# Performance work log

Hardware: AMD Instinct MI355X
Metric: run time of the kernel (lower is better)

The kernel has to match this reference:

```python
import jax, jax.numpy as jnp
import numpy as np

NUM_HEADS = 8
NEG_MASK = -1000.0  # original code masks with -1000, not -inf


def setup_inputs() -> dict:
    key = jax.random.key(0)
    ks = jax.random.split(key, 12)
    B, S, D = 4, 2048, 512
    HID, OUT = 512, 512
    dh = D // NUM_HEADS      # 64, per-head input dim
    eh = HID // NUM_HEADS    # 64, per-head hidden dim
    w = 0.02
    return {
        "q": jax.random.normal(ks[0], (B, S, D), dtype=jnp.float32),
        "k": jax.random.normal(ks[1], (B, S, D), dtype=jnp.float32),
        "v": jax.random.normal(ks[2], (B, S, D), dtype=jnp.float32),
        # Linear weights stored as [in, out] (transpose of torch convention)
        "Wq": jax.random.normal(ks[3], (dh, eh), dtype=jnp.float32) * w,
        "bq": jax.random.normal(ks[4], (eh,), dtype=jnp.float32) * w,
        "Wk": jax.random.normal(ks[5], (dh, eh), dtype=jnp.float32) * w,
        "bk": jax.random.normal(ks[6], (eh,), dtype=jnp.float32) * w,
        "Wv": jax.random.normal(ks[7], (dh, eh), dtype=jnp.float32) * w,
        "bv": jax.random.normal(ks[8], (eh,), dtype=jnp.float32) * w,
        "Wo": jax.random.normal(ks[9], (HID, OUT), dtype=jnp.float32) * w,
        "bo": jax.random.normal(ks[10], (OUT,), dtype=jnp.float32) * w,
        "valid_lens": jnp.maximum(jax.random.randint(ks[11], (B,), 0, S), 1),
        "max_len": S,
    }


def reference(q, k, v, Wq, bq, Wk, bk, Wv, bv, Wo, bo, valid_lens, max_len):
    B, S, D = q.shape
    H = NUM_HEADS
    # split into heads: [B, S, H, dh]; note the SAME projection weights are
    # shared across heads (as in the original module)
    qh = q.reshape(B, S, H, D // H)
    kh = k.reshape(B, S, H, D // H)
    vh = v.reshape(B, S, H, D // H)
    qp = jnp.einsum('bshd,de->bshe', qh, Wq) + bq  # [B,S,H,eh]
    kp = jnp.einsum('bshd,de->bshe', kh, Wk) + bk
    vp = jnp.einsum('bshd,de->bshe', vh, Wv) + bv
    scale = 1.0 / jnp.sqrt(jnp.asarray(qp.shape[-1], qp.dtype))
    scores = jnp.einsum('bshe,bthe->bhst', qp, kp) * scale  # [B,H,S,S]
    # key-padding mask: positions j >= valid_len get -1000 (original semantics)
    key_mask = jnp.arange(S)[None, :] < valid_lens[:, None]  # [B,S]
    scores = jnp.where(key_mask[:, None, None, :], scores, NEG_MASK)
    attn = jax.nn.softmax(scores, axis=-1)
    ctx = jnp.einsum('bhst,bthe->bshe', attn, vp).reshape(B, S, -1)  # head-major concat
    return jnp.einsum('bse,eo->bso', ctx, Wo) + bo
```

## Files before the change

kernel.cpp:

```cpp
#include <hip/hip_runtime.h>

#define S_LEN 2048
#define D_MODEL 512

typedef __attribute__((ext_vector_type(8))) short s8v;
typedef __attribute__((ext_vector_type(4))) float f4v;
typedef __attribute__((ext_vector_type(4))) short s4v;
typedef __attribute__((ext_vector_type(4))) int   i4v;
typedef __attribute__((ext_vector_type(2))) int   i2v;

#define MFMA __builtin_amdgcn_mfma_f32_16x16x32_bf16

__device__ inline short f2bf(float x) {
    union { float f; unsigned u; } v; v.f = x;
    unsigned r = v.u + 0x7fffu + ((v.u >> 16) & 1u);
    return (short)(r >> 16);
}
__device__ inline unsigned pack_bf2_trunc(float a, float b) {
    unsigned ua = __builtin_bit_cast(unsigned, a);
    unsigned ub = __builtin_bit_cast(unsigned, b);
    return (ua >> 16) | (ub & 0xffff0000u);
}

template <int C>
__device__ inline float dppf(float x) {
    int i = __builtin_bit_cast(int, x);
    i = __builtin_amdgcn_update_dpp(0, i, C, 0xF, 0xF, true);
    return __builtin_bit_cast(float, i);
}
__device__ inline float rowsum16(float x) {
    x += dppf<0xB1>(x);
    x += dppf<0x4E>(x);
    x += dppf<0x141>(x);
    x += dppf<0x140>(x);
    return x;
}

typedef const __attribute__((address_space(1))) void* gptr_t;
typedef __attribute__((address_space(3))) void* sptr_t;
__device__ inline void gload16(const void* g, void* s) {
    __builtin_amdgcn_global_load_lds((gptr_t)g, (sptr_t)s, 16, 0, 0);
}

__global__ __launch_bounds__(256) void prep_kernel(
    const float* __restrict__ Wo, short* __restrict__ WoT)
{
    __shared__ short t[64 * 65];
    const int bi = (blockIdx.x >> 3) * 64;
    const int bj = (blockIdx.x & 7) * 64;
    const int c = threadIdx.x & 63, rr = threadIdx.x >> 6;
#pragma unroll
    for (int r = 0; r < 16; r++) {
        int i = r * 4 + rr;
        t[c * 65 + i] = f2bf(Wo[(size_t)(bi + i) * 512 + bj + c]);
    }
    __syncthreads();
#pragma unroll
    for (int r = 0; r < 16; r++) {
        int o = r * 4 + rr;
        WoT[(size_t)(bj + o) * 512 + bi + c] = t[o * 65 + c];
    }
}

__global__ __launch_bounds__(256) void proj_kernel(
    const float* __restrict__ q, const float* __restrict__ k, const float* __restrict__ v,
    const float* __restrict__ Wq, const float* __restrict__ Wk, const float* __restrict__ Wv,
    const float* __restrict__ bq, const float* __restrict__ bk, const float* __restrict__ bv,
    short* __restrict__ qp, short* __restrict__ kfrag, short* __restrict__ vfrag)
{
    __shared__ short sm[128 * 64];

    const int t = blockIdx.z >> 2;
    const int b = blockIdx.z & 3;
    const int h = blockIdx.y;
    const int qt = blockIdx.x;
    const int w = threadIdx.x >> 6, lane = threadIdx.x & 63;
    const int l = lane & 15, qd = lane >> 4;

    const float* X    = (t == 0) ? q  : (t == 1) ? k  : v;
    const float* Wp   = (t == 0) ? Wq : (t == 1) ? Wk : Wv;
    const float* bias = (t == 0) ? bq : (t == 1) ? bk : bv;

    {
        const int d = threadIdx.x >> 2, c4 = threadIdx.x & 3;
        const float* src = Wp + d * 64 + c4 * 16;
        f4v x0 = *(const f4v*)(src);
        f4v x1 = *(const f4v*)(src + 4);
        f4v x2 = *(const f4v*)(src + 8);
        f4v x3 = *(const f4v*)(src + 12);
        float xs[16] = {x0[0],x0[1],x0[2],x0[3], x1[0],x1[1],x1[2],x1[3],
                        x2[0],x2[1],x2[2],x2[3], x3[0],x3[1],x3[2],x3[3]};
#pragma unroll
        for (int j = 0; j < 16; j++) {
            int e = c4 * 16 + j;
            int sidx = (e * 64 + d) ^ (((e >> 2) & 7) << 3);
            sm[sidx] = f2bf(xs[j]);
        }
    }
    __syncthreads();

    const int s0 = qt * 128 + w * 32;

    s8v a[2][2];
#pragma unroll
    for (int mt = 0; mt < 2; mt++)
#pragma unroll
        for (int kk = 0; kk < 2; kk++) {
            const float* p = X + (size_t)(b * S_LEN + s0 + mt * 16 + l) * 512 + h * 64 + kk * 32 + qd * 8;
            f4v x0 = *(const f4v*)p;
            f4v x1 = *(const f4v*)(p + 4);
            s8v fr;
            fr[0] = f2bf(x0[0]); fr[1] = f2bf(x0[1]); fr[2] = f2bf(x0[2]); fr[3] = f2bf(x0[3]);
            fr[4] = f2bf(x1[0]); fr[5] = f2bf(x1[1]); fr[6] = f2bf(x1[2]); fr[7] = f2bf(x1[3]);
            a[mt][kk] = fr;
        }
    s8v wf[4][2];
#pragma unroll
    for (int nt = 0; nt < 4; nt++) {
        int wrow = (t < 2) ? (4 * l + nt) : (nt * 16 + l);
        int key = ((wrow >> 2) & 7) << 3;
#pragma unroll
        for (int kk = 0; kk < 2; kk++)
            wf[nt][kk] = *(const s8v*)(sm + ((wrow * 64 + kk * 32 + qd * 8) ^ key));
    }

    const f4v fz = {0.f, 0.f, 0.f, 0.f};
    f4v acc[2][4];
#pragma unroll
    for (int mt = 0; mt < 2; mt++)
#pragma unroll
        for (int nt = 0; nt < 4; nt++) acc[mt][nt] = fz;

#pragma unroll
    for (int kk = 0; kk < 2; kk++)
#pragma unroll
        for (int nt = 0; nt < 4; nt++)
#pragma unroll
            for (int mt = 0; mt < 2; mt++)
                acc[mt][nt] = MFMA(a[mt][kk], wf[nt][kk], acc[mt][nt], 0, 0, 0);

    const float SC = 0.125f * 1.442695041f;

    if (t == 0) {
        float bbs[4];
#pragma unroll
        for (int nt = 0; nt < 4; nt++) bbs[nt] = bias[4 * l + nt];
#pragma unroll
        for (int mt = 0; mt < 2; mt++)
#pragma unroll
            for (int r = 0; r < 4; r++) {
                int s = s0 + mt * 16 + qd * 4 + r;
                s4v pk;
#pragma unroll
                for (int nt = 0; nt < 4; nt++)
                    pk[nt] = f2bf((acc[mt][nt][r] + bbs[nt]) * SC);
                *(s4v*)(qp + ((size_t)(b * 8 + h) * S_LEN + s) * 64 + 4 * l) = pk;
            }
        return;
    }

    __syncthreads();

    if (t == 1) {
        float bbs[4];
#pragma unroll
        for (int nt = 0; nt < 4; nt++) bbs[nt] = bias[4 * l + nt];
#pragma unroll
        for (int mt = 0; mt < 2; mt++)
#pragma unroll
            for (int r = 0; r < 4; r++) {
                int sl = w * 32 + mt * 16 + qd * 4 + r;
                s4v pk;
#pragma unroll
                for (int nt = 0; nt < 4; nt++) pk[nt] = f2bf(acc[mt][nt][r] + bbs[nt]);
                int sidx = (sl * 64 + 4 * l) ^ (((sl >> 2) & 7) << 3);
                *(s4v*)(sm + sidx) = pk;
            }
    } else {
#pragma unroll
        for (int nt = 0; nt < 4; nt++) {
            float bb = bias[nt * 16 + l];
            int e = nt * 16 + l;
            int key = ((e >> 2) & 7) << 3;
#pragma unroll
            for (int mt = 0; mt < 2; mt++) {
                s4v pk;
#pragma unroll
                for (int r = 0; r < 4; r++) pk[r] = f2bf(acc[mt][nt][r] + bb);
                int sidx = (e * 128 + w * 32 + mt * 16 + qd * 4) ^ key;
                *(s4v*)(sm + sidx) = pk;
            }
        }
    }
    __syncthreads();

    short* dst = (t == 1) ? kfrag : vfrag;
    const size_t obase0 = ((size_t)(b * 8 + h) * 32 + qt * 2) * 4096;
    const int f = threadIdx.x & 63, cp = threadIdx.x >> 6;
    const int fl = f & 15, fq = f >> 4;
#pragma unroll
    for (int tt = 0; tt < 2; tt++)
#pragma unroll
        for (int ci = 0; ci < 2; ci++) {
            int c = cp + ci * 4;
            int n2 = c >> 1, kk = c & 1;
            int sidx;
            if (t == 1) {
                int sl = tt * 64 + 4 * fl + n2;
                sidx = (sl * 64 + kk * 32 + fq * 8) ^ (((sl >> 2) & 7) << 3);
            } else {
                int e = 4 * fl + n2;
                sidx = (e * 128 + tt * 64 + kk * 32 + fq * 8) ^ (((e >> 2) & 7) << 3);
            }
            s8v x = *(const s8v*)(sm + sidx);
            *(s8v*)(dst + obase0 + tt * 4096 + c * 512 + f * 8) = x;
        }
}

__global__ __launch_bounds__(256, 3) void attn_kernel(
    const short* __restrict__ qp, const short* __restrict__ kfrag,
    const short* __restrict__ vfrag,
    const int* __restrict__ valid_lens, short* __restrict__ ctx)
{
    __shared__ alignas(16) short kbuf[2][4096];
    __shared__ alignas(16) short lP[4][32 * 72];

    const int gid = blockIdx.x;
    const int h  = gid & 7;
    int b        = (gid >> 3) & 3;
    const int qt = gid >> 5;
    b ^= 3 * ((gid >> 8) & 1);
    const int w = threadIdx.x >> 6, lane = threadIdx.x & 63;
    const int l = lane & 15, qd = lane >> 4;
    const int vlen = valid_lens[b];
    const int ntiles = (vlen + 63) >> 6;

    const int bh = b * 8 + h;
    const short* Qs = qp + (size_t)bh * S_LEN * 64;
    const short* Kf = kfrag + (size_t)bh * 32 * 4096;
    const short* Vf = vfrag + (size_t)bh * 32 * 4096;

    const int s0 = qt * 128 + w * 32;
    s8v qf[2][2];
#pragma unroll
    for (int mt = 0; mt < 2; mt++)
#pragma unroll
        for (int kk = 0; kk < 2; kk++)
            qf[mt][kk] = *(const s8v*)(Qs + (size_t)(s0 + mt * 16 + l) * 64 + kk * 32 + qd * 8);

    const f4v fz = {0.f, 0.f, 0.f, 0.f};
    f4v O[2][4];
    float lsum[2][4];
#pragma unroll
    for (int mt = 0; mt < 2; mt++)
#pragma unroll
        for (int r = 0; r < 4; r++) lsum[mt][r] = 0.f;
#pragma unroll
    for (int mt = 0; mt < 2; mt++)
#pragma unroll
        for (int ne = 0; ne < 4; ne++) O[mt][ne] = fz;

    short* lPw = lP[w];
    const int toff = threadIdx.x * 8;

    gload16(Kf + toff,        &kbuf[0][toff]);
    gload16(Kf + 2048 + toff, &kbuf[0][2048 + toff]);
    __syncthreads();

    for (int kb = 0; kb < ntiles; kb++) {
        const int cur = kb & 1;
        if (kb + 1 < ntiles) {
            const short* Ks = Kf + (size_t)(kb + 1) * 4096;
            gload16(Ks + toff,        &kbuf[cur ^ 1][toff]);
            gload16(Ks + 2048 + toff, &kbuf[cur ^ 1][2048 + toff]);
        }

        const short* Vb = Vf + (size_t)kb * 4096 + lane * 8;
        s8v vf[4][2];
#pragma unroll
        for (int ne = 0; ne < 4; ne++)
#pragma unroll
            for (int kk = 0; kk < 2; kk++)
                vf[ne][kk] = *(const s8v*)(Vb + (ne * 2 + kk) * 512);

        const short* Kb = &kbuf[cur][lane * 8];
        s8v kf[4][2];
#pragma unroll
        for (int nt = 0; nt < 4; nt++)
#pragma unroll
            for (int kk = 0; kk < 2; kk++)
                kf[nt][kk] = *(const s8v*)(Kb + (nt * 2 + kk) * 512);

        f4v sf[2][4];
#pragma unroll
        for (int mt = 0; mt < 2; mt++)
#pragma unroll
            for (int nt = 0; nt < 4; nt++) sf[mt][nt] = fz;
        __builtin_amdgcn_s_setprio(1);
#pragma unroll
        for (int nt = 0; nt < 4; nt++)
#pragma unroll
            for (int mt = 0; mt < 2; mt++) {
                sf[mt][nt] = MFMA(qf[mt][0], kf[nt][0], sf[mt][nt], 0, 0, 0);
                sf[mt][nt] = MFMA(qf[mt][1], kf[nt][1], sf[mt][nt], 0, 0, 0);
            }
        __builtin_amdgcn_s_setprio(0);

        if (kb == ntiles - 1 && (vlen & 63)) {
            int rem = vlen - kb * 64;
#pragma unroll
            for (int nt = 0; nt < 4; nt++)
                if (4 * l + nt >= rem) {
#pragma unroll
                    for (int mt = 0; mt < 2; mt++)
#pragma unroll
                        for (int r = 0; r < 4; r++) sf[mt][nt][r] = -1e30f;
                }
        }

#pragma unroll
        for (int mt = 0; mt < 2; mt++)
#pragma unroll
            for (int r = 0; r < 4; r++) {
                float p0 = __builtin_amdgcn_exp2f(sf[mt][0][r]);
                float p1 = __builtin_amdgcn_exp2f(sf[mt][1][r]);
                float p2 = __builtin_amdgcn_exp2f(sf[mt][2][r]);
                float p3 = __builtin_amdgcn_exp2f(sf[mt][3][r]);
                lsum[mt][r] += (p0 + p1) + (p2 + p3);
                i2v pk;
                pk[0] = (int)pack_bf2_trunc(p0, p1);
                pk[1] = (int)pack_bf2_trunc(p2, p3);
                *(i2v*)(lPw + (mt * 16 + qd * 4 + r) * 72 + 4 * l) = pk;
            }

        s8v pa[2][2];
#pragma unroll
        for (int mt = 0; mt < 2; mt++)
#pragma unroll
            for (int kk = 0; kk < 2; kk++)
                pa[mt][kk] = *(const s8v*)(lPw + (mt * 16 + l) * 72 + kk * 32 + qd * 8);
        __builtin_amdgcn_s_setprio(1);
#pragma unroll
        for (int ne = 0; ne < 4; ne++)
#pragma unroll
            for (int mt = 0; mt < 2; mt++) {
                O[mt][ne] = MFMA(pa[mt][0], vf[ne][0], O[mt][ne], 0, 0, 0);
                O[mt][ne] = MFMA(pa[mt][1], vf[ne][1], O[mt][ne], 0, 0, 0);
            }
        __builtin_amdgcn_s_setprio(0);

        __syncthreads();
    }

#pragma unroll
    for (int mt = 0; mt < 2; mt++)
#pragma unroll
        for (int r = 0; r < 4; r++) {
            float inv = 1.0f / rowsum16(lsum[mt][r]);
            int s = s0 + mt * 16 + qd * 4 + r;
            s4v pk;
#pragma unroll
            for (int ne = 0; ne < 4; ne++) pk[ne] = f2bf(O[mt][ne][r] * inv);
            *(s4v*)(ctx + ((size_t)(b * S_LEN + s)) * 512 + h * 64 + 4 * l) = pk;
        }
}

__global__ __launch_bounds__(256) void outproj_kernel(
    const short* __restrict__ ctx, const short* __restrict__ WoT,
    const float* __restrict__ bo, float* __restrict__ out)
{
    __shared__ short lB[64 * 520];
    __shared__ short lA[128 * 40];

    const int rb = blockIdx.x * 128;
    const int nb = blockIdx.y * 64;
    const int w = threadIdx.x >> 6, lane = threadIdx.x & 63;
    const int l = lane & 15, qd = lane >> 4;

    {
        int n = threadIdx.x >> 2, c0 = threadIdx.x & 3;
#pragma unroll
        for (int i = 0; i < 16; i++) {
            int g = i * 4 + c0;
            i4v x = *(const i4v*)(WoT + (size_t)(nb + n) * 512 + g * 8);
            *(i4v*)(lB + n * 520 + g * 8) = x;
        }
    }
    __syncthreads();

    const f4v fz = {0.f, 0.f, 0.f, 0.f};
    f4v acc[2][4];
#pragma unroll
    for (int mt = 0; mt < 2; mt++)
#pragma unroll
        for (int nt = 0; nt < 4; nt++) acc[mt][nt] = fz;

    for (int ko = 0; ko < 16; ko++) {
        {
            int r = threadIdx.x >> 1, hp = threadIdx.x & 1;
            const short* src = ctx + (size_t)(rb + r) * 512 + ko * 32 + hp * 16;
            i4v x0 = *(const i4v*)src;
            i4v x1 = *(const i4v*)(src + 8);
            *(i4v*)(lA + r * 40 + hp * 16) = x0;
            *(i4v*)(lA + r * 40 + hp * 16 + 8) = x1;
        }
        __syncthreads();
        s8v af[2];
#pragma unroll
        for (int mt = 0; mt < 2; mt++)
            af[mt] = *(const s8v*)(lA + (w * 32 + mt * 16 + l) * 40 + qd * 8);
#pragma unroll
        for (int nt = 0; nt < 4; nt++) {
            s8v bfr = *(const s8v*)(lB + (nt * 16 + l) * 520 + ko * 32 + qd * 8);
#pragma unroll
            for (int mt = 0; mt < 2; mt++)
                acc[mt][nt] = MFMA(af[mt], bfr, acc[mt][nt], 0, 0, 0);
        }
        __syncthreads();
    }

#pragma unroll
    for (int nt = 0; nt < 4; nt++) {
        float bias = bo[nb + nt * 16 + l];
#pragma unroll
        for (int mt = 0; mt < 2; mt++)
#pragma unroll
            for (int r = 0; r < 4; r++) {
                int row = rb + w * 32 + mt * 16 + qd * 4 + r;
                out[(size_t)row * 512 + nb + nt * 16 + l] = acc[mt][nt][r] + bias;
            }
    }
}

extern "C" void kernel_launch(void* const* d_in, const int* in_sizes, int n_in,
                              void* d_out, int out_size, void* d_ws, size_t ws_size,
                              hipStream_t stream)
{
    const float* q  = (const float*)d_in[0];
    const float* k  = (const float*)d_in[1];
    const float* v  = (const float*)d_in[2];
    const float* Wq = (const float*)d_in[3];
    const float* bq = (const float*)d_in[4];
    const float* Wk = (const float*)d_in[5];
    const float* bk = (const float*)d_in[6];
    const float* Wv = (const float*)d_in[7];
    const float* bv = (const float*)d_in[8];
    const float* Wo = (const float*)d_in[9];
    const float* bo = (const float*)d_in[10];
    const int*   vl = (const int*)d_in[11];
    float* out = (float*)d_out;

    char* ws = (char*)d_ws;
    const size_t SL = (size_t)4 * 8 * S_LEN * 64 * sizeof(short);
    short* qp    = (short*)(ws);
    short* ctx   = (short*)(ws + SL);
    short* kfrag = (short*)(ws + 2 * SL);
    short* vfrag = (short*)(ws + 3 * SL);
    short* WoT   = (short*)(ws + 4 * SL);

    prep_kernel<<<64, 256, 0, stream>>>(Wo, WoT);
    proj_kernel<<<dim3(16, 8, 12), 256, 0, stream>>>(q, k, v, Wq, Wk, Wv,
                                                     bq, bk, bv, qp, kfrag, vfrag);
    attn_kernel<<<512, 256, 0, stream>>>(qp, kfrag, vfrag, vl, ctx);
    outproj_kernel<<<dim3(64, 8), 256, 0, stream>>>(ctx, WoT, bo, out);
}
```

Measured before the change: 167.5 us.

## Software-pipeline PV MFMA one tile behind QK with double-buffered P

Restructures the attention loop so the P·V MFMAs for the previous key tile are issued together with the current tile's QK^T MFMAs. The P tile is double-buffered in shared memory per wave, and a tail step handles the last tile. V fragments are loaded after the MFMAs, so they are in flight during the exp/softmax step. Occupancy hint drops from 3 to 2 blocks per CU to make room for the extra live registers and LDS, which trades parallelism for instruction-level overlap.

```diff
diff --git a/kernel.cpp b/kernel.cpp
--- a/kernel.cpp
+++ b/kernel.cpp
@@ -217,13 +217,13 @@
         }
 }
 
-__global__ __launch_bounds__(256, 3) void attn_kernel(
+__global__ __launch_bounds__(256, 2) void attn_kernel(
     const short* __restrict__ qp, const short* __restrict__ kfrag,
     const short* __restrict__ vfrag,
     const int* __restrict__ valid_lens, short* __restrict__ ctx)
 {
     __shared__ alignas(16) short kbuf[2][4096];
-    __shared__ alignas(16) short lP[4][32 * 72];
+    __shared__ alignas(16) short lP[4][2][32 * 72];
 
     const int gid = blockIdx.x;
     const int h  = gid & 7;
@@ -260,12 +260,13 @@
 #pragma unroll
         for (int ne = 0; ne < 4; ne++) O[mt][ne] = fz;
 
-    short* lPw = lP[w];
     const int toff = threadIdx.x * 8;
 
     gload16(Kf + toff,        &kbuf[0][toff]);
     gload16(Kf + 2048 + toff, &kbuf[0][2048 + toff]);
     __syncthreads();
+
+    s8v vf[4][2];
 
     for (int kb = 0; kb < ntiles; kb++) {
         const int cur = kb & 1;
@@ -275,14 +276,6 @@
             gload16(Ks + 2048 + toff, &kbuf[cur ^ 1][2048 + toff]);
         }
 
-        const short* Vb = Vf + (size_t)kb * 4096 + lane * 8;
-        s8v vf[4][2];
-#pragma unroll
-        for (int ne = 0; ne < 4; ne++)
-#pragma unroll
-            for (int kk = 0; kk < 2; kk++)
-                vf[ne][kk] = *(const s8v*)(Vb + (ne * 2 + kk) * 512);
-
         const short* Kb = &kbuf[cur][lane * 8];
         s8v kf[4][2];
 #pragma unroll
@@ -290,6 +283,16 @@
 #pragma unroll
             for (int kk = 0; kk < 2; kk++)
                 kf[nt][kk] = *(const s8v*)(Kb + (nt * 2 + kk) * 512);
+
+        s8v pa[2][2];
+        if (kb > 0) {
+            const short* lPr = lP[w][cur ^ 1];
+#pragma unroll
+            for (int mt = 0; mt < 2; mt++)
+#pragma unroll
+                for (int kk = 0; kk < 2; kk++)
+                    pa[mt][kk] = *(const s8v*)(lPr + (mt * 16 + l) * 72 + kk * 32 + qd * 8);
+        }
 
         f4v sf[2][4];
 #pragma unroll
@@ -304,7 +307,23 @@
                 sf[mt][nt] = MFMA(qf[mt][0], kf[nt][0], sf[mt][nt], 0, 0, 0);
                 sf[mt][nt] = MFMA(qf[mt][1], kf[nt][1], sf[mt][nt], 0, 0, 0);
             }
+        if (kb > 0) {
+#pragma unroll
+            for (int ne = 0; ne < 4; ne++)
+#pragma unroll
+                for (int mt = 0; mt < 2; mt++) {
+                    O[mt][ne] = MFMA(pa[mt][0], vf[ne][0], O[mt][ne], 0, 0, 0);
+                    O[mt][ne] = MFMA(pa[mt][1], vf[ne][1], O[mt][ne], 0, 0, 0);
+                }
+        }
         __builtin_amdgcn_s_setprio(0);
+
+        const short* Vb = Vf + (size_t)kb * 4096 + lane * 8;
+#pragma unroll
+        for (int ne = 0; ne < 4; ne++)
+#pragma unroll
+            for (int kk = 0; kk < 2; kk++)
+                vf[ne][kk] = *(const s8v*)(Vb + (ne * 2 + kk) * 512);
 
         if (kb == ntiles - 1 && (vlen & 63)) {
             int rem = vlen - kb * 64;
@@ -318,28 +337,35 @@
                 }
         }
 
-#pragma unroll
-        for (int mt = 0; mt < 2; mt++)
-#pragma unroll
-            for (int r = 0; r < 4; r++) {
-                float p0 = __builtin_amdgcn_exp2f(sf[mt][0][r]);
-                float p1 = __builtin_amdgcn_exp2f(sf[mt][1][r]);
-                float p2 = __builtin_amdgcn_exp2f(sf[mt][2][r]);
-                float p3 = __builtin_amdgcn_exp2f(sf[mt][3][r]);
-                lsum[mt][r] += (p0 + p1) + (p2 + p3);
-                i2v pk;
-                pk[0] = (int)pack_bf2_trunc(p0, p1);
-                pk[1] = (int)pack_bf2_trunc(p2, p3);
-                *(i2v*)(lPw + (mt * 16 + qd * 4 + r) * 72 + 4 * l) = pk;
-            }
-
+        {
+            short* lPwr = lP[w][cur];
+#pragma unroll
+            for (int mt = 0; mt < 2; mt++)
+#pragma unroll
+                for (int r = 0; r < 4; r++) {
+                    float p0 = __builtin_amdgcn_exp2f(sf[mt][0][r]);
+                    float p1 = __builtin_amdgcn_exp2f(sf[mt][1][r]);
+                    float p2 = __builtin_amdgcn_exp2f(sf[mt][2][r]);
+                    float p3 = __builtin_amdgcn_exp2f(sf[mt][3][r]);
+                    lsum[mt][r] += (p0 + p1) + (p2 + p3);
+                    i2v pk;
+                    pk[0] = (int)pack_bf2_trunc(p0, p1);
+                    pk[1] = (int)pack_bf2_trunc(p2, p3);
+                    *(i2v*)(lPwr + (mt * 16 + qd * 4 + r) * 72 + 4 * l) = pk;
+                }
+        }
+
+        __syncthreads();
+    }
+
+    {
+        const short* lPr = lP[w][(ntiles - 1) & 1];
         s8v pa[2][2];
 #pragma unroll
         for (int mt = 0; mt < 2; mt++)
 #pragma unroll
             for (int kk = 0; kk < 2; kk++)
-                pa[mt][kk] = *(const s8v*)(lPw + (mt * 16 + l) * 72 + kk * 32 + qd * 8);
-        __builtin_amdgcn_s_setprio(1);
+                pa[mt][kk] = *(const s8v*)(lPr + (mt * 16 + l) * 72 + kk * 32 + qd * 8);
 #pragma unroll
         for (int ne = 0; ne < 4; ne++)
 #pragma unroll
@@ -347,9 +373,6 @@
                 O[mt][ne] = MFMA(pa[mt][0], vf[ne][0], O[mt][ne], 0, 0, 0);
                 O[mt][ne] = MFMA(pa[mt][1], vf[ne][1], O[mt][ne], 0, 0, 0);
             }
-        __builtin_amdgcn_s_setprio(0);
-
-        __syncthreads();
     }
 
 #pragma unroll
```

New measurement: 168.8 us. Within noise of the previous version (+0.8%).

## Process two 64-key subtiles per barrier with 128-key double-buffered K staging

Applied to the files above, without the earlier changes.

The attention loop now stages 128 keys of K per pipeline step instead of 64 and runs two 64-key subtiles between each pair of __syncthreads, which halves the number of block-wide barriers and K prefetch rounds. The LDS K buffer doubles in size, and occupancy bounds drop from 3 to 2 blocks per CU. Masking of the tail subtile moves to the last outer iteration. A subtile past vlen can still be processed when vlen rounds to an odd count of 64-key tiles. It is fully masked, so it adds wasted work and possible out-of-range K/V reads.

```diff
diff --git a/kernel.cpp b/kernel.cpp
--- a/kernel.cpp
+++ b/kernel.cpp
@@ -217,12 +217,12 @@
         }
 }
 
-__global__ __launch_bounds__(256, 3) void attn_kernel(
+__global__ __launch_bounds__(256, 2) void attn_kernel(
     const short* __restrict__ qp, const short* __restrict__ kfrag,
     const short* __restrict__ vfrag,
     const int* __restrict__ valid_lens, short* __restrict__ ctx)
 {
-    __shared__ alignas(16) short kbuf[2][4096];
+    __shared__ alignas(16) short kbuf[2][8192];
     __shared__ alignas(16) short lP[4][32 * 72];
 
     const int gid = blockIdx.x;
@@ -233,7 +233,7 @@
     const int w = threadIdx.x >> 6, lane = threadIdx.x & 63;
     const int l = lane & 15, qd = lane >> 4;
     const int vlen = valid_lens[b];
-    const int ntiles = (vlen + 63) >> 6;
+    const int nt2 = (vlen + 127) >> 7;
 
     const int bh = b * 8 + h;
     const short* Qs = qp + (size_t)bh * S_LEN * 64;
@@ -263,91 +263,100 @@
     short* lPw = lP[w];
     const int toff = threadIdx.x * 8;
 
-    gload16(Kf + toff,        &kbuf[0][toff]);
-    gload16(Kf + 2048 + toff, &kbuf[0][2048 + toff]);
-    __syncthreads();
-
-    for (int kb = 0; kb < ntiles; kb++) {
-        const int cur = kb & 1;
-        if (kb + 1 < ntiles) {
-            const short* Ks = Kf + (size_t)(kb + 1) * 4096;
-            gload16(Ks + toff,        &kbuf[cur ^ 1][toff]);
-            gload16(Ks + 2048 + toff, &kbuf[cur ^ 1][2048 + toff]);
-        }
-
-        const short* Vb = Vf + (size_t)kb * 4096 + lane * 8;
-        s8v vf[4][2];
-#pragma unroll
-        for (int ne = 0; ne < 4; ne++)
-#pragma unroll
-            for (int kk = 0; kk < 2; kk++)
-                vf[ne][kk] = *(const s8v*)(Vb + (ne * 2 + kk) * 512);
-
-        const short* Kb = &kbuf[cur][lane * 8];
-        s8v kf[4][2];
-#pragma unroll
-        for (int nt = 0; nt < 4; nt++)
-#pragma unroll
-            for (int kk = 0; kk < 2; kk++)
-                kf[nt][kk] = *(const s8v*)(Kb + (nt * 2 + kk) * 512);
-
-        f4v sf[2][4];
-#pragma unroll
-        for (int mt = 0; mt < 2; mt++)
-#pragma unroll
-            for (int nt = 0; nt < 4; nt++) sf[mt][nt] = fz;
-        __builtin_amdgcn_s_setprio(1);
-#pragma unroll
-        for (int nt = 0; nt < 4; nt++)
-#pragma unroll
-            for (int mt = 0; mt < 2; mt++) {
-                sf[mt][nt] = MFMA(qf[mt][0], kf[nt][0], sf[mt][nt], 0, 0, 0);
-                sf[mt][nt] = MFMA(qf[mt][1], kf[nt][1], sf[mt][nt], 0, 0, 0);
-            }
-        __builtin_amdgcn_s_setprio(0);
-
-        if (kb == ntiles - 1 && (vlen & 63)) {
-            int rem = vlen - kb * 64;
+#pragma unroll
+    for (int r = 0; r < 4; r++)
+        gload16(Kf + r * 2048 + toff, &kbuf[0][r * 2048 + toff]);
+    __syncthreads();
+
+    for (int j = 0; j < nt2; j++) {
+        const int cur = j & 1;
+        if (j + 1 < nt2) {
+            const short* Ks = Kf + (size_t)(j + 1) * 8192;
+#pragma unroll
+            for (int r = 0; r < 4; r++)
+                gload16(Ks + r * 2048 + toff, &kbuf[cur ^ 1][r * 2048 + toff]);
+        }
+
+#pragma unroll
+        for (int st = 0; st < 2; st++) {
+            const int kb = 2 * j + st;
+
+            const short* Vb = Vf + (size_t)kb * 4096 + lane * 8;
+            s8v vf[4][2];
+#pragma unroll
+            for (int ne = 0; ne < 4; ne++)
+#pragma unroll
+                for (int kk = 0; kk < 2; kk++)
+                    vf[ne][kk] = *(const s8v*)(Vb + (ne * 2 + kk) * 512);
+
+            const short* Kb = &kbuf[cur][st * 4096 + lane * 8];
+            s8v kf[4][2];
 #pragma unroll
             for (int nt = 0; nt < 4; nt++)
-                if (4 * l + nt >= rem) {
-#pragma unroll
-                    for (int mt = 0; mt < 2; mt++)
-#pragma unroll
-                        for (int r = 0; r < 4; r++) sf[mt][nt][r] = -1e30f;
+#pragma unroll
+                for (int kk = 0; kk < 2; kk++)
+                    kf[nt][kk] = *(const s8v*)(Kb + (nt * 2 + kk) * 512);
+
+            f4v sf[2][4];
+#pragma unroll
+            for (int mt = 0; mt < 2; mt++)
+#pragma unroll
+                for (int nt = 0; nt < 4; nt++) sf[mt][nt] = fz;
+            __builtin_amdgcn_s_setprio(1);
+#pragma unroll
+            for (int nt = 0; nt < 4; nt++)
+#pragma unroll
+                for (int mt = 0; mt < 2; mt++) {
+                    sf[mt][nt] = MFMA(qf[mt][0], kf[nt][0], sf[mt][nt], 0, 0, 0);
+                    sf[mt][nt] = MFMA(qf[mt][1], kf[nt][1], sf[mt][nt], 0, 0, 0);
                 }
-        }
-
-#pragma unroll
-        for (int mt = 0; mt < 2; mt++)
-#pragma unroll
-            for (int r = 0; r < 4; r++) {
-                float p0 = __builtin_amdgcn_exp2f(sf[mt][0][r]);
-                float p1 = __builtin_amdgcn_exp2f(sf[mt][1][r]);
-                float p2 = __builtin_amdgcn_exp2f(sf[mt][2][r]);
-                float p3 = __builtin_amdgcn_exp2f(sf[mt][3][r]);
-                lsum[mt][r] += (p0 + p1) + (p2 + p3);
-                i2v pk;
-                pk[0] = (int)pack_bf2_trunc(p0, p1);
-                pk[1] = (int)pack_bf2_trunc(p2, p3);
-                *(i2v*)(lPw + (mt * 16 + qd * 4 + r) * 72 + 4 * l) = pk;
-            }
-
-        s8v pa[2][2];
-#pragma unroll
-        for (int mt = 0; mt < 2; mt++)
-#pragma unroll
-            for (int kk = 0; kk < 2; kk++)
-                pa[mt][kk] = *(const s8v*)(lPw + (mt * 16 + l) * 72 + kk * 32 + qd * 8);
-        __builtin_amdgcn_s_setprio(1);
-#pragma unroll
-        for (int ne = 0; ne < 4; ne++)
-#pragma unroll
-            for (int mt = 0; mt < 2; mt++) {
-                O[mt][ne] = MFMA(pa[mt][0], vf[ne][0], O[mt][ne], 0, 0, 0);
-                O[mt][ne] = MFMA(pa[mt][1], vf[ne][1], O[mt][ne], 0, 0, 0);
-            }
-        __builtin_amdgcn_s_setprio(0);
+            __builtin_amdgcn_s_setprio(0);
+
+            if (j == nt2 - 1) {
+                int rem = vlen - kb * 64;
+                if (rem < 64) {
+#pragma unroll
+                    for (int nt = 0; nt < 4; nt++)
+                        if (4 * l + nt >= rem) {
+#pragma unroll
+                            for (int mt = 0; mt < 2; mt++)
+#pragma unroll
+                                for (int r = 0; r < 4; r++) sf[mt][nt][r] = -1e30f;
+                        }
+                }
+            }
+
+#pragma unroll
+            for (int mt = 0; mt < 2; mt++)
+#pragma unroll
+                for (int r = 0; r < 4; r++) {
+                    float p0 = __builtin_amdgcn_exp2f(sf[mt][0][r]);
+                    float p1 = __builtin_amdgcn_exp2f(sf[mt][1][r]);
+                    float p2 = __builtin_amdgcn_exp2f(sf[mt][2][r]);
+                    float p3 = __builtin_amdgcn_exp2f(sf[mt][3][r]);
+                    lsum[mt][r] += (p0 + p1) + (p2 + p3);
+                    i2v pk;
+                    pk[0] = (int)pack_bf2_trunc(p0, p1);
+                    pk[1] = (int)pack_bf2_trunc(p2, p3);
+                    *(i2v*)(lPw + (mt * 16 + qd * 4 + r) * 72 + 4 * l) = pk;
+                }
+
+            s8v pa[2][2];
+#pragma unroll
+            for (int mt = 0; mt < 2; mt++)
+#pragma unroll
+                for (int kk = 0; kk < 2; kk++)
+                    pa[mt][kk] = *(const s8v*)(lPw + (mt * 16 + l) * 72 + kk * 32 + qd * 8);
+            __builtin_amdgcn_s_setprio(1);
+#pragma unroll
+            for (int ne = 0; ne < 4; ne++)
+#pragma unroll
+                for (int mt = 0; mt < 2; mt++) {
+                    O[mt][ne] = MFMA(pa[mt][0], vf[ne][0], O[mt][ne], 0, 0, 0);
+                    O[mt][ne] = MFMA(pa[mt][1], vf[ne][1], O[mt][ne], 0, 0, 0);
+                }
+            __builtin_amdgcn_s_setprio(0);
+        }
 
         __syncthreads();
     }
```

Result: no change. 164.9 us (-1.6%).
